# Optimization experiments

Measured on AMD Instinct MI355X. Metric: run time of the kernel, lower is better.

## Reference

```python
import jax, jax.numpy as jnp
import numpy as np

B, T, D, H, LAT = 512, 8, 512, 512, 64
NSTEPS = 4  # fixed RK4 steps per observation interval (replaces adaptive dopri5)


def _lin(key, out_dim, in_dim):
    k1, k2 = jax.random.split(key)
    s = 1.0 / np.sqrt(in_dim)
    W = jax.random.uniform(k1, (out_dim, in_dim), minval=-s, maxval=s, dtype=jnp.float32)
    b = jax.random.uniform(k2, (out_dim,), minval=-s, maxval=s, dtype=jnp.float32)
    return W, b


def setup_inputs() -> dict:
    key = jax.random.key(0)
    ks = jax.random.split(key, 8)
    x = jax.random.normal(ks[0], (B, T, D), dtype=jnp.float32)
    # strictly increasing per-sample observation times
    ts = jnp.cumsum(jax.random.uniform(ks[1], (B, T), dtype=jnp.float32) + 0.05, axis=1)
    Wih, bih = _lin(ks[2], 3 * H, D)      # GRU input weights
    Whh, bhh = _lin(ks[3], 3 * H, H)      # GRU hidden weights
    Wout, bout = _lin(ks[4], 2 * LAT, H)  # h2o head: mean/logvar of latent
    W1, b1 = _lin(ks[5], 2 * H, H + 1)    # LatentODEfunc fc1 (state + time)
    W2, b2 = _lin(ks[6], 2 * H, 2 * H)    # fc2
    W3, b3 = _lin(ks[7], H, 2 * H)        # fc3
    return dict(x=x, ts=ts, Wih=Wih, Whh=Whh, bih=bih, bhh=bhh,
                Wout=Wout, bout=bout, W1=W1, b1=b1, W2=W2, b2=b2, W3=W3, b3=b3)


def reference(x, ts, Wih, Whh, bih, bhh, Wout, bout, W1, b1, W2, b2, W3, b3):
    swish = lambda v: v * jax.nn.sigmoid(v)

    def odefunc(t, h):  # t: (B,), h: (B,H) -> dh/dt (B,H)
        z = jnp.concatenate([h, t[:, None]], axis=1)
        z = swish(z @ W1.T + b1)
        z = swish(z @ W2.T + b2)
        return z @ W3.T + b3

    def ode_integrate(h, t0, t1):  # batched RK4 with per-sample dt
        dt = (t1 - t0) / NSTEPS  # (B,)
        def body(carry, _):
            h, t = carry
            d = dt[:, None]
            k1 = odefunc(t, h)
            k2 = odefunc(t + dt / 2, h + d * k1 / 2)
            k3 = odefunc(t + dt / 2, h + d * k2 / 2)
            k4 = odefunc(t + dt, h + d * k3)
            return (h + d / 6 * (k1 + 2 * k2 + 2 * k3 + k4), t + dt), None
        (h, _), _ = jax.lax.scan(body, (h, t0), None, length=NSTEPS)
        return h

    def gru_cell(obs, h):  # torch GRUCell math
        gi = obs @ Wih.T + bih
        gh = h @ Whh.T + bhh
        ir, iz, inn = jnp.split(gi, 3, axis=1)
        hr, hz, hn = jnp.split(gh, 3, axis=1)
        r = jax.nn.sigmoid(ir + hr)
        zg = jax.nn.sigmoid(iz + hz)
        n = jnp.tanh(inn + r * hn)
        return (1.0 - zg) * n + zg * h

    # first interval has zero length -> RK4 with dt=0 leaves h0 unchanged (no ODE at t=0)
    t_prev = jnp.concatenate([ts[:, :1], ts[:, :-1]], axis=1)

    def step(carry, inputs):
        h, c = carry
        obs, t0, t1 = inputs
        h = ode_integrate(h, t0, t1)
        h = gru_cell(obs, h)
        out = h @ Wout.T + bout  # (B, 2*LAT)
        return (h, c), out

    h0 = jnp.zeros((x.shape[0], H), x.dtype)
    c0 = jnp.zeros_like(h0)
    xs = (jnp.swapaxes(x, 0, 1), t_prev.T, ts.T)  # time-major for scan
    (h, c), outs = jax.lax.scan(step, (h0, c0), xs)
    return outs[-1], h, c
```

## Files before the change

### kernel.cpp

```cpp
#include <hip/hip_runtime.h>
#include <hip/hip_bf16.h>
#include <stdint.h>


#define B_ 512
#define T_ 8
#define H_ 512
#define D_ 512

typedef short short8 __attribute__((ext_vector_type(8)));
typedef float f32x4 __attribute__((ext_vector_type(4)));
typedef __hip_bfloat16 bf16;
typedef unsigned long long u64;

__device__ __forceinline__ float sigm(float x){ return 1.f/(1.f+__expf(-x)); }

#define MFMA16(a,b,c) __builtin_amdgcn_mfma_f32_16x16x32_bf16((a),(b),(c),0,0,0)
#define ALD4(p)   __hip_atomic_load((p), __ATOMIC_RELAXED, __HIP_MEMORY_SCOPE_AGENT)
#define AST8(p,v) __hip_atomic_store((u64*)(p),(v),__ATOMIC_RELAXED,__HIP_MEMORY_SCOPE_AGENT)

__device__ __forceinline__ void wait_ge(unsigned* c, unsigned tgt, int* dead){
  if (threadIdx.x == 0){
    if (!*dead){
      int it = 0;
      while (ALD4(c) < tgt){
        __builtin_amdgcn_s_sleep(1);
        if (++it > 50000000){ *dead = 1; break; }
      }
    }
  }
  __syncthreads();
}
__device__ __forceinline__ void publish(unsigned* c){
  __builtin_amdgcn_s_waitcnt(0);
  __syncthreads();
  if (threadIdx.x == 0)
    __hip_atomic_fetch_add(c, 1u, __ATOMIC_RELAXED, __HIP_MEMORY_SCOPE_AGENT);
}

template<int CH, int SH>
__device__ __forceinline__ void stageC16(bf16* lds, int lstr, const bf16* g, int gstr){
  f32x4 tmp[CH];
#pragma unroll
  for (int j = 0; j < CH; ++j){
    int idx = j*256 + threadIdx.x;
    const bf16* p = g + (size_t)(idx >> SH)*gstr + (size_t)(idx & ((1<<SH)-1))*8;
    asm volatile("global_load_dwordx4 %0, %1, off sc0 sc1" : "=v"(tmp[j]) : "v"(p));
  }
  asm volatile("s_waitcnt vmcnt(0)" ::: "memory");
  __builtin_amdgcn_sched_barrier(0);
#pragma unroll
  for (int j = 0; j < CH; ++j){
    int idx = j*256 + threadIdx.x;
    *(f32x4*)&lds[(idx >> SH)*lstr + (idx & ((1<<SH)-1))*8] = tmp[j];
  }
}
template<int CH, int SH>
__device__ __forceinline__ void stageP(bf16* lds, int lstr, const bf16* g, size_t gstr){
#pragma unroll
  for (int j = 0; j < CH; ++j){
    int idx = j*256 + threadIdx.x;
    *(short8*)&lds[(idx >> SH)*lstr + (idx & ((1<<SH)-1))*8] =
        *(const short8*)(g + (size_t)(idx >> SH)*gstr + (size_t)(idx & ((1<<SH)-1))*8);
  }
}

__device__ __forceinline__ u64 pk4(float a0, float a1, float a2, float a3){
  union { bf16 h[4]; u64 q; } u;
  u.h[0] = __float2bfloat16(a0); u.h[1] = __float2bfloat16(a1);
  u.h[2] = __float2bfloat16(a2); u.h[3] = __float2bfloat16(a3);
  return u.q;
}

__global__ __launch_bounds__(256, 1) void persist_k(
    const bf16* __restrict__ W1hb, const bf16* __restrict__ W2b,
    const bf16* __restrict__ W3b,  const bf16* __restrict__ Woutb,
    const bf16* __restrict__ Wc3,  const bf16* __restrict__ xbf,
    const float* __restrict__ b1,  const float* __restrict__ b2,
    const float* __restrict__ b3,  const float* __restrict__ bout,
    const float* __restrict__ bcb3,const float* __restrict__ w1t,
    const float* __restrict__ ts,
    bf16* wbuf, bf16* z1buf, bf16* z2buf,
    unsigned* cnts, float* dout)
{
  extern __shared__ char smem[];
  bf16* slab = (bf16*)smem;
  bf16* W3s  = (bf16*)(smem + 66048);
  float* t0s = (float*)(smem + 132096);
  float* dts = t0s + 32;
  float* tcs = dts + 32;
  int* dead  = (int*)(smem + 132480);

  const int tid = threadIdx.x, lane = tid & 63, wv = tid >> 6;
  const int fr = lane & 15, quad = lane >> 4;
  const int nb = blockIdx.x & 15;
  const int mb = blockIdx.x >> 4;
  const int gm0 = mb * 32;
  const int wm = wv & 1;
  const int wn = wv >> 1;

  unsigned* cz1 = cnts + mb*128;
  unsigned* cz2 = cz1 + 32;
  unsigned* cw  = cz1 + 64;
  unsigned* cgt = cz1 + 96;

  stageP<16,7>(W3s, 1032, W3b + (size_t)(32*nb)*1024, 1024);
  if (tid < 32){
    float t0 = ts[(gm0 + tid)*T_];
    t0s[tid] = t0; tcs[tid] = t0; dts[tid] = 0.f;
  }
  if (tid == 0) *dead = 0;
  __syncthreads();

  const int zc0 = 64*nb + 16*wv + quad*4;
  const int kc0 = 32*nb + 16*wn + quad*4;
  const f32x4 b1v  = *(const f32x4*)&b1[zc0];
  const f32x4 w1tv = *(const f32x4*)&w1t[zc0];
  const f32x4 b2v  = *(const f32x4*)&b2[zc0];
  const f32x4 b3v  = *(const f32x4*)&b3[kc0];
  f32x4 bcv[4];
#pragma unroll
  for (int g = 0; g < 4; ++g)
    bcv[g] = *(const f32x4*)&bcb3[nb*128 + g*32 + 16*wn + quad*4];
  const f32x4 bov = *(const f32x4*)&bout[16*(nb & 7) + quad*4];

  const bf16* w1p = W1hb  + (size_t)(64*nb + 16*wv + fr)*512  + quad*8;
  const bf16* w2p = W2b   + (size_t)(64*nb + 16*wv + fr)*1024 + quad*8;
  const bf16* wop = Woutb + (size_t)(16*(nb & 7) + fr)*512 + quad*8;
  const bf16* wcp[4];
#pragma unroll
  for (int g = 0; g < 4; ++g)
    wcp[g] = Wc3 + (size_t)(nb*128 + g*32 + 16*wn + fr)*1024 + quad*8;

  short8 w1f[16], w2f[32];
#pragma unroll
  for (int k = 0; k < 16; ++k) w1f[k] = *(const short8*)(w1p + k*32);
#pragma unroll
  for (int k = 0; k < 32; ++k) w2f[k] = *(const short8*)(w2p + k*32);

  float hreg[4] = {0,0,0,0}, kacc[4] = {0,0,0,0};
  unsigned tz1 = 16, tz2 = 16, tw = 16, tg = 16;

  for (int s = 0; s < T_; ++s){
    for (int sub = 0; sub < 4; ++sub){
      for (int e = 1; e <= 4; ++e){
        wait_ge(cw, tw, dead);
        stageC16<8,6>(slab, 520, wbuf + (size_t)gm0*512, 512);
        __syncthreads();
        {
          f32x4 a0 = {0,0,0,0}, a1 = {0,0,0,0};
#pragma unroll
          for (int k = 0; k < 16; ++k){
            a0 = MFMA16(w1f[k], *(const short8*)&slab[fr*520      + k*32 + quad*8], a0);
            a1 = MFMA16(w1f[k], *(const short8*)&slab[(16+fr)*520 + k*32 + quad*8], a1);
          }
          float t0v = tcs[fr], t1v = tcs[16 + fr];
          float s0[4], s1[4];
#pragma unroll
          for (int j = 0; j < 4; ++j){
            float v0 = a0[j] + b1v[j] + t0v*w1tv[j];
            float v1 = a1[j] + b1v[j] + t1v*w1tv[j];
            s0[j] = v0*sigm(v0); s1[j] = v1*sigm(v1);
          }
          AST8(z1buf + (size_t)(gm0 + fr)*1024 + zc0,      pk4(s0[0],s0[1],s0[2],s0[3]));
          AST8(z1buf + (size_t)(gm0 + 16 + fr)*1024 + zc0, pk4(s1[0],s1[1],s1[2],s1[3]));
          publish(cz1);
        }
        wait_ge(cz1, tz1, dead); tz1 += 16;
        stageC16<16,7>(slab, 1032, z1buf + (size_t)gm0*1024, 1024);
        __syncthreads();
        {
          f32x4 a0 = {0,0,0,0}, a1 = {0,0,0,0};
#pragma unroll
          for (int k = 0; k < 32; ++k){
            a0 = MFMA16(w2f[k], *(const short8*)&slab[fr*1032      + k*32 + quad*8], a0);
            a1 = MFMA16(w2f[k], *(const short8*)&slab[(16+fr)*1032 + k*32 + quad*8], a1);
          }
          float s0[4], s1[4];
#pragma unroll
          for (int j = 0; j < 4; ++j){
            float v0 = a0[j] + b2v[j], v1 = a1[j] + b2v[j];
            s0[j] = v0*sigm(v0); s1[j] = v1*sigm(v1);
          }
          AST8(z2buf + (size_t)(gm0 + fr)*1024 + zc0,      pk4(s0[0],s0[1],s0[2],s0[3]));
          AST8(z2buf + (size_t)(gm0 + 16 + fr)*1024 + zc0, pk4(s1[0],s1[1],s1[2],s1[3]));
          publish(cz2);
        }
        wait_ge(cz2, tz2, dead); tz2 += 16;
        stageC16<16,7>(slab, 1032, z2buf + (size_t)gm0*1024, 1024);
        __syncthreads();
        {
          f32x4 ak = {0,0,0,0};
#pragma unroll 8
          for (int k = 0; k < 32; ++k){
            ak = MFMA16(*(const short8*)&W3s[(16*wn + fr)*1032 + k*32 + quad*8],
                        *(const short8*)&slab[(wm*16 + fr)*1032 + k*32 + quad*8], ak);
          }
          const int r = wm*16 + fr;
          const float dtv = dts[r];
          float w4[4];
#pragma unroll
          for (int j = 0; j < 4; ++j){
            float v = ak[j] + b3v[j];
            float ka = (e == 1) ? v : kacc[j] + ((e == 4) ? 1.f : 2.f)*v;
            if (e < 4){ kacc[j] = ka; w4[j] = hreg[j] + ((e == 3) ? 1.f : 0.5f)*dtv*v; }
            else      { hreg[j] = hreg[j] + dtv*(1.f/6.f)*ka; w4[j] = hreg[j]; }
          }
          AST8(wbuf + (size_t)(gm0 + r)*512 + kc0, pk4(w4[0],w4[1],w4[2],w4[3]));
          if (tid < 32){
            float ce = (e <= 2) ? ((float)sub + 0.5f) : ((float)sub + 1.f);
            tcs[tid] = t0s[tid] + dts[tid]*ce;
          }
          publish(cw); tw += 16;
        }
      }
    }
    wait_ge(cw, tw, dead);
    stageC16<8,6>(slab, 1032, wbuf + (size_t)gm0*512, 512);
    stageP<8,6>(slab + 512, 1032, xbf + ((size_t)gm0*T_ + s)*512, (size_t)T_*512);
    __syncthreads();
    publish(cgt);
    {
      f32x4 ag[4] = {{0,0,0,0},{0,0,0,0},{0,0,0,0},{0,0,0,0}};
#pragma unroll 4
      for (int k = 0; k < 32; ++k){
        short8 xv = *(const short8*)&slab[(wm*16 + fr)*1032 + k*32 + quad*8];
#pragma unroll
        for (int g = 0; g < 4; ++g)
          ag[g] = MFMA16(*(const short8*)(wcp[g] + k*32), xv, ag[g]);
      }
      wait_ge(cgt, tg, dead); tg += 16;
      const int r = wm*16 + fr;
#pragma unroll
      for (int j = 0; j < 4; ++j){
        float r_ = sigm(ag[0][j] + bcv[0][j]);
        float z_ = sigm(ag[1][j] + bcv[1][j]);
        float hn = ag[2][j] + bcv[2][j];
        float in = ag[3][j] + bcv[3][j];
        float n_ = tanhf(in + r_*hn);
        hreg[j] = (1.f - z_)*n_ + z_*hreg[j];
      }
      AST8(wbuf + (size_t)(gm0 + r)*512 + kc0, pk4(hreg[0],hreg[1],hreg[2],hreg[3]));
      if (tid < 32){
        float t0n = ts[(gm0 + tid)*T_ + s];
        float t1  = (s < T_-1) ? ts[(gm0 + tid)*T_ + s + 1] : t0n;
        t0s[tid] = t0n; tcs[tid] = t0n; dts[tid] = (t1 - t0n)*0.25f;
      }
      publish(cw); tw += 16;
    }
  }
  wait_ge(cw, tw, dead);
  stageC16<8,6>(slab, 520, wbuf + (size_t)gm0*512, 512);
  __syncthreads();
  if (nb < 8 && wv < 2){
    f32x4 ao = {0,0,0,0};
#pragma unroll 4
    for (int k = 0; k < 16; ++k){
      ao = MFMA16(*(const short8*)(wop + k*32),
                  *(const short8*)&slab[(wv*16 + fr)*520 + k*32 + quad*8], ao);
    }
    f32x4 o;
#pragma unroll
    for (int j = 0; j < 4; ++j) o[j] = ao[j] + bov[j];
    *(f32x4*)&dout[(size_t)(gm0 + wv*16 + fr)*128 + 16*nb + quad*4] = o;
  }
  {
    const int r = wm*16 + fr;
    f32x4 hv; hv[0]=hreg[0]; hv[1]=hreg[1]; hv[2]=hreg[2]; hv[3]=hreg[3];
    *(f32x4*)&dout[(size_t)B_*128 + (size_t)(gm0 + r)*512 + kc0] = hv;
    f32x4 z4 = {0,0,0,0};
    *(f32x4*)&dout[(size_t)B_*128 + (size_t)B_*512 + (size_t)(gm0 + r)*512 + kc0] = z4;
  }
}

__global__ void conv_k(const float* __restrict__ in, bf16* __restrict__ out,
                       int rows, int kin, int kout)
{
  int idx = blockIdx.x*256 + threadIdx.x;
  if (idx >= rows*kout) return;
  int r = idx / kout, k = idx - r*kout;
  out[idx] = __float2bfloat16(k < kin ? in[(size_t)r*kin + k] : 0.f);
}

__global__ void w1t_k(const float* __restrict__ W1, float* __restrict__ w1t)
{
  int i = blockIdx.x*256 + threadIdx.x;
  if (i < 1024) w1t[i] = W1[(size_t)i*513 + 512];
}

__global__ void wc3_k(const float* __restrict__ Wih, const float* __restrict__ Whh,
                      const float* __restrict__ bih, const float* __restrict__ bhh,
                      bf16* __restrict__ Wc3, float* __restrict__ bcb3)
{
  int idx = blockIdx.x*256 + threadIdx.x;
  if (idx >= 2048*1024) return;
  int R = idx >> 10, k = idx & 1023;
  int n16 = R >> 7, g = (R >> 5) & 3, c = R & 31;
  int hc = n16*32 + c;
  float v;
  if      (g == 0) v = (k < 512) ? Whh[(size_t)hc*512 + k]        : Wih[(size_t)hc*512 + k - 512];
  else if (g == 1) v = (k < 512) ? Whh[(size_t)(512+hc)*512 + k]  : Wih[(size_t)(512+hc)*512 + k - 512];
  else if (g == 2) v = (k < 512) ? Whh[(size_t)(1024+hc)*512 + k] : 0.f;
  else             v = (k < 512) ? 0.f                             : Wih[(size_t)(1024+hc)*512 + k - 512];
  Wc3[idx] = __float2bfloat16(v);
  if (k == 0){
    if      (g == 0) bcb3[R] = bih[hc] + bhh[hc];
    else if (g == 1) bcb3[R] = bih[512 + hc] + bhh[512 + hc];
    else if (g == 2) bcb3[R] = bhh[1024 + hc];
    else             bcb3[R] = bih[1024 + hc];
  }
}

__global__ void init_k(bf16* __restrict__ wbuf, unsigned* __restrict__ cnts)
{
  int idx = blockIdx.x*256 + threadIdx.x;
  if (idx < B_*H_) wbuf[idx] = __float2bfloat16(0.f);
  if (idx < 16*128){
    int off = idx & 127;
    cnts[idx] = (off == 64) ? 16u : 0u;
  }
}

extern "C" void kernel_launch(void* const* d_in, const int* in_sizes, int n_in,
                              void* d_out, int out_size, void* d_ws, size_t ws_size,
                              hipStream_t stream)
{
  const float* x    = (const float*)d_in[0];
  const float* ts   = (const float*)d_in[1];
  const float* Wih  = (const float*)d_in[2];
  const float* Whh  = (const float*)d_in[3];
  const float* bih  = (const float*)d_in[4];
  const float* bhh  = (const float*)d_in[5];
  const float* Wout = (const float*)d_in[6];
  const float* bout = (const float*)d_in[7];
  const float* W1   = (const float*)d_in[8];
  const float* b1   = (const float*)d_in[9];
  const float* W2   = (const float*)d_in[10];
  const float* b2   = (const float*)d_in[11];
  const float* W3   = (const float*)d_in[12];
  const float* b3   = (const float*)d_in[13];

  char* ws = (char*)d_ws;
  size_t off = 0;
  auto alloc = [&](size_t n){ void* p = ws + off; off += (n + 255) & ~(size_t)255; return p; };

  bf16* xbf   = (bf16*)alloc((size_t)B_*T_*D_*2);
  bf16* W1hb  = (bf16*)alloc((size_t)1024*512*2);
  bf16* W2b   = (bf16*)alloc((size_t)1024*1024*2);
  bf16* W3b   = (bf16*)alloc((size_t)512*1024*2);
  bf16* Woutb = (bf16*)alloc((size_t)128*512*2);
  bf16* Wc3   = (bf16*)alloc((size_t)2048*1024*2);
  float* bcb3 = (float*)alloc((size_t)2048*4);
  float* w1t  = (float*)alloc((size_t)1024*4);
  bf16* wbuf  = (bf16*)alloc((size_t)B_*H_*2);
  bf16* z1buf = (bf16*)alloc((size_t)B_*1024*2);
  bf16* z2buf = (bf16*)alloc((size_t)B_*1024*2);
  unsigned* cnts = (unsigned*)alloc((size_t)16*128*4);

  auto conv = [&](const float* in, bf16* out, int rows, int kin, int kout){
    int n = rows*kout;
    conv_k<<<(n + 255)/256, 256, 0, stream>>>(in, out, rows, kin, kout);
  };
  conv(x, xbf, B_*T_, D_, D_);
  conv(W1, W1hb, 1024, 513, 512);
  conv(W2, W2b, 1024, 1024, 1024);
  conv(W3, W3b, 512, 1024, 1024);
  conv(Wout, Woutb, 128, 512, 512);
  w1t_k<<<4, 256, 0, stream>>>(W1, w1t);
  wc3_k<<<(2048*1024)/256, 256, 0, stream>>>(Wih, Whh, bih, bhh, Wc3, bcb3);
  init_k<<<(B_*H_ + 255)/256, 256, 0, stream>>>(wbuf, cnts);

  (void)hipFuncSetAttribute((const void*)persist_k,
                            hipFuncAttributeMaxDynamicSharedMemorySize, 132608);
  persist_k<<<256, 256, 132608, stream>>>(
      W1hb, W2b, W3b, Woutb, Wc3, xbf,
      b1, b2, b3, bout, bcb3, w1t, ts,
      wbuf, z1buf, z2buf, cnts, (float*)d_out);
}
```

Before: 1.903 ms.

## Fold W3 into W1 so each RK4 stage chains fc2 to fused Wf=W1·W3

Precomputes Wf = W1[:, :H]·W3 and bf3 = W1·b3 so the next stage's fc1 pre-activation comes straight from z2 via one GEMM, removing the separate fc3 GEMM and its grid-wide sync phase per RK4 stage. The h state is tracked in fc1-projected space, and fc3 is applied once per interval to the weighted z2 sum. This cuts the barrier phases per stage from three to two but makes the per-stage GEMM K=1024 instead of 512, uses more register-resident weights, and changes bf16 rounding paths, which may affect accuracy.

```diff
diff --git a/kernel.cpp b/kernel.cpp
--- a/kernel.cpp
+++ b/kernel.cpp
@@ -74,22 +74,21 @@
 
 __global__ __launch_bounds__(256, 1) void persist_k(
     const bf16* __restrict__ W1hb, const bf16* __restrict__ W2b,
-    const bf16* __restrict__ W3b,  const bf16* __restrict__ Woutb,
-    const bf16* __restrict__ Wc3,  const bf16* __restrict__ xbf,
+    const bf16* __restrict__ Wfb,  const bf16* __restrict__ W3b,
+    const bf16* __restrict__ Woutb,const bf16* __restrict__ Wc3,
+    const bf16* __restrict__ xbf,
     const float* __restrict__ b1,  const float* __restrict__ b2,
     const float* __restrict__ b3,  const float* __restrict__ bout,
     const float* __restrict__ bcb3,const float* __restrict__ w1t,
-    const float* __restrict__ ts,
-    bf16* wbuf, bf16* z1buf, bf16* z2buf,
+    const float* __restrict__ bf3, const float* __restrict__ ts,
+    bf16* wbuf, bf16* hbuf, bf16* z1buf, bf16* z2buf, bf16* zbuf,
     unsigned* cnts, float* dout)
 {
   extern __shared__ char smem[];
   bf16* slab = (bf16*)smem;
-  bf16* W3s  = (bf16*)(smem + 66048);
-  float* t0s = (float*)(smem + 132096);
-  float* dts = t0s + 32;
-  float* tcs = dts + 32;
-  int* dead  = (int*)(smem + 132480);
+  float* t0s = (float*)(smem + 66048);
+  float* dts = (float*)(smem + 66176);
+  int* dead  = (int*)(smem + 66304);
 
   const int tid = threadIdx.x, lane = tid & 63, wv = tid >> 6;
   const int fr = lane & 15, quad = lane >> 4;
@@ -101,13 +100,12 @@
 
   unsigned* cz1 = cnts + mb*128;
   unsigned* cz2 = cz1 + 32;
-  unsigned* cw  = cz1 + 64;
-  unsigned* cgt = cz1 + 96;
-
-  stageP<16,7>(W3s, 1032, W3b + (size_t)(32*nb)*1024, 1024);
+  unsigned* ch  = cz1 + 64;
+  unsigned* cg  = cz1 + 96;
+
   if (tid < 32){
     float t0 = ts[(gm0 + tid)*T_];
-    t0s[tid] = t0; tcs[tid] = t0; dts[tid] = 0.f;
+    t0s[tid] = t0; dts[tid] = 0.f;
   }
   if (tid == 0) *dead = 0;
   __syncthreads();
@@ -117,6 +115,7 @@
   const f32x4 b1v  = *(const f32x4*)&b1[zc0];
   const f32x4 w1tv = *(const f32x4*)&w1t[zc0];
   const f32x4 b2v  = *(const f32x4*)&b2[zc0];
+  const f32x4 bf3v = *(const f32x4*)&bf3[zc0];
   const f32x4 b3v  = *(const f32x4*)&b3[kc0];
   f32x4 bcv[4];
 #pragma unroll
@@ -126,46 +125,43 @@
 
   const bf16* w1p = W1hb  + (size_t)(64*nb + 16*wv + fr)*512  + quad*8;
   const bf16* w2p = W2b   + (size_t)(64*nb + 16*wv + fr)*1024 + quad*8;
+  const bf16* wfp = Wfb   + (size_t)(64*nb + 16*wv + fr)*1024 + quad*8;
+  const bf16* w3p = W3b   + (size_t)(32*nb + 16*wn + fr)*1024 + quad*8;
   const bf16* wop = Woutb + (size_t)(16*(nb & 7) + fr)*512 + quad*8;
   const bf16* wcp[4];
 #pragma unroll
   for (int g = 0; g < 4; ++g)
     wcp[g] = Wc3 + (size_t)(nb*128 + g*32 + 16*wn + fr)*1024 + quad*8;
 
-  short8 w1f[16], w2f[32];
-#pragma unroll
-  for (int k = 0; k < 16; ++k) w1f[k] = *(const short8*)(w1p + k*32);
+  short8 w2f[32], wff[32];
 #pragma unroll
   for (int k = 0; k < 32; ++k) w2f[k] = *(const short8*)(w2p + k*32);
-
-  float hreg[4] = {0,0,0,0}, kacc[4] = {0,0,0,0};
-  unsigned tz1 = 16, tz2 = 16, tw = 16, tg = 16;
+#pragma unroll
+  for (int k = 0; k < 32; ++k) wff[k] = *(const short8*)(wfp + k*32);
+
+  float hw0[4]={0,0,0,0}, hw1[4]={0,0,0,0};
+  float pacc0[4]={0,0,0,0}, pacc1[4]={0,0,0,0};
+  float zacc0[4]={0,0,0,0}, zacc1[4]={0,0,0,0};
+  float hreg[4]={0,0,0,0};
+  unsigned tz1 = 16, tz2 = 16, tch = 16, tcg = 16;
+
+  {
+    const float t0a = t0s[fr], t0b = t0s[16 + fr];
+    float v0[4], v1[4];
+#pragma unroll
+    for (int j = 0; j < 4; ++j){
+      v0[j] = t0a*w1tv[j] + b1v[j];
+      v1[j] = t0b*w1tv[j] + b1v[j];
+      v0[j] *= sigm(v0[j]); v1[j] *= sigm(v1[j]);
+    }
+    AST8(z1buf + (size_t)(gm0 + fr)*1024 + zc0,      pk4(v0[0],v0[1],v0[2],v0[3]));
+    AST8(z1buf + (size_t)(gm0 + 16 + fr)*1024 + zc0, pk4(v1[0],v1[1],v1[2],v1[3]));
+    publish(cz1);
+  }
 
   for (int s = 0; s < T_; ++s){
     for (int sub = 0; sub < 4; ++sub){
       for (int e = 1; e <= 4; ++e){
-        wait_ge(cw, tw, dead);
-        stageC16<8,6>(slab, 520, wbuf + (size_t)gm0*512, 512);
-        __syncthreads();
-        {
-          f32x4 a0 = {0,0,0,0}, a1 = {0,0,0,0};
-#pragma unroll
-          for (int k = 0; k < 16; ++k){
-            a0 = MFMA16(w1f[k], *(const short8*)&slab[fr*520      + k*32 + quad*8], a0);
-            a1 = MFMA16(w1f[k], *(const short8*)&slab[(16+fr)*520 + k*32 + quad*8], a1);
-          }
-          float t0v = tcs[fr], t1v = tcs[16 + fr];
-          float s0[4], s1[4];
-#pragma unroll
-          for (int j = 0; j < 4; ++j){
-            float v0 = a0[j] + b1v[j] + t0v*w1tv[j];
-            float v1 = a1[j] + b1v[j] + t1v*w1tv[j];
-            s0[j] = v0*sigm(v0); s1[j] = v1*sigm(v1);
-          }
-          AST8(z1buf + (size_t)(gm0 + fr)*1024 + zc0,      pk4(s0[0],s0[1],s0[2],s0[3]));
-          AST8(z1buf + (size_t)(gm0 + 16 + fr)*1024 + zc0, pk4(s1[0],s1[1],s1[2],s1[3]));
-          publish(cz1);
-        }
         wait_ge(cz1, tz1, dead); tz1 += 16;
         stageC16<16,7>(slab, 1032, z1buf + (size_t)gm0*1024, 1024);
         __syncthreads();
@@ -176,50 +172,92 @@
             a0 = MFMA16(w2f[k], *(const short8*)&slab[fr*1032      + k*32 + quad*8], a0);
             a1 = MFMA16(w2f[k], *(const short8*)&slab[(16+fr)*1032 + k*32 + quad*8], a1);
           }
+          const float wgt = (e == 2 || e == 3) ? 2.f : 1.f;
           float s0[4], s1[4];
 #pragma unroll
           for (int j = 0; j < 4; ++j){
             float v0 = a0[j] + b2v[j], v1 = a1[j] + b2v[j];
             s0[j] = v0*sigm(v0); s1[j] = v1*sigm(v1);
+            zacc0[j] += wgt*s0[j]; zacc1[j] += wgt*s1[j];
           }
-          AST8(z2buf + (size_t)(gm0 + fr)*1024 + zc0,      pk4(s0[0],s0[1],s0[2],s0[3]));
-          AST8(z2buf + (size_t)(gm0 + 16 + fr)*1024 + zc0, pk4(s1[0],s1[1],s1[2],s1[3]));
+          if (sub == 3 && e == 4){
+            AST8(zbuf + (size_t)(gm0 + fr)*1024 + zc0,      pk4(zacc0[0],zacc0[1],zacc0[2],zacc0[3]));
+            AST8(zbuf + (size_t)(gm0 + 16 + fr)*1024 + zc0, pk4(zacc1[0],zacc1[1],zacc1[2],zacc1[3]));
+#pragma unroll
+            for (int j = 0; j < 4; ++j){ zacc0[j] = 0.f; zacc1[j] = 0.f; }
+          } else {
+            AST8(z2buf + (size_t)(gm0 + fr)*1024 + zc0,      pk4(s0[0],s0[1],s0[2],s0[3]));
+            AST8(z2buf + (size_t)(gm0 + 16 + fr)*1024 + zc0, pk4(s1[0],s1[1],s1[2],s1[3]));
+          }
           publish(cz2);
         }
-        wait_ge(cz2, tz2, dead); tz2 += 16;
-        stageC16<16,7>(slab, 1032, z2buf + (size_t)gm0*1024, 1024);
-        __syncthreads();
-        {
-          f32x4 ak = {0,0,0,0};
+        if (!(sub == 3 && e == 4)){
+          wait_ge(cz2, tz2, dead); tz2 += 16;
+          stageC16<16,7>(slab, 1032, z2buf + (size_t)gm0*1024, 1024);
+          __syncthreads();
+          f32x4 p0 = {0,0,0,0}, p1 = {0,0,0,0};
+#pragma unroll
+          for (int k = 0; k < 32; ++k){
+            p0 = MFMA16(wff[k], *(const short8*)&slab[fr*1032      + k*32 + quad*8], p0);
+            p1 = MFMA16(wff[k], *(const short8*)&slab[(16+fr)*1032 + k*32 + quad*8], p1);
+          }
+          const float dta = dts[fr], dtb = dts[16 + fr];
+          const float t0a = t0s[fr], t0b = t0s[16 + fr];
+          const float ce = (e <= 2) ? (float)sub + 0.5f : (float)sub + 1.f;
+          float v0[4], v1[4];
+          if (e < 4){
+            const float c = (e == 3) ? 1.f : 0.5f;
+            const float wgt = (e == 2 || e == 3) ? 2.f : 1.f;
+            if (sub < 3){
+#pragma unroll
+              for (int j = 0; j < 4; ++j){ pacc0[j] += wgt*p0[j]; pacc1[j] += wgt*p1[j]; }
+            }
+#pragma unroll
+            for (int j = 0; j < 4; ++j){
+              v0[j] = hw0[j] + c*dta*(p0[j] + bf3v[j]) + (t0a + dta*ce)*w1tv[j] + b1v[j];
+              v1[j] = hw1[j] + c*dtb*(p1[j] + bf3v[j]) + (t0b + dtb*ce)*w1tv[j] + b1v[j];
+            }
+          } else {
+#pragma unroll
+            for (int j = 0; j < 4; ++j){
+              float pa = pacc0[j] + p0[j], pb = pacc1[j] + p1[j];
+              hw0[j] += dta*(1.f/6.f)*pa + dta*bf3v[j];
+              hw1[j] += dtb*(1.f/6.f)*pb + dtb*bf3v[j];
+              pacc0[j] = 0.f; pacc1[j] = 0.f;
+              v0[j] = hw0[j] + (t0a + dta*ce)*w1tv[j] + b1v[j];
+              v1[j] = hw1[j] + (t0b + dtb*ce)*w1tv[j] + b1v[j];
+            }
+          }
+#pragma unroll
+          for (int j = 0; j < 4; ++j){ v0[j] *= sigm(v0[j]); v1[j] *= sigm(v1[j]); }
+          AST8(z1buf + (size_t)(gm0 + fr)*1024 + zc0,      pk4(v0[0],v0[1],v0[2],v0[3]));
+          AST8(z1buf + (size_t)(gm0 + 16 + fr)*1024 + zc0, pk4(v1[0],v1[1],v1[2],v1[3]));
+          publish(cz1);
+        }
+      }
+    }
+    wait_ge(cz2, tz2, dead); tz2 += 16;
+    stageC16<16,7>(slab, 1032, zbuf + (size_t)gm0*1024, 1024);
+    __syncthreads();
+    {
+      f32x4 ak = {0,0,0,0};
 #pragma unroll 8
-          for (int k = 0; k < 32; ++k){
-            ak = MFMA16(*(const short8*)&W3s[(16*wn + fr)*1032 + k*32 + quad*8],
-                        *(const short8*)&slab[(wm*16 + fr)*1032 + k*32 + quad*8], ak);
-          }
-          const int r = wm*16 + fr;
-          const float dtv = dts[r];
-          float w4[4];
-#pragma unroll
-          for (int j = 0; j < 4; ++j){
-            float v = ak[j] + b3v[j];
-            float ka = (e == 1) ? v : kacc[j] + ((e == 4) ? 1.f : 2.f)*v;
-            if (e < 4){ kacc[j] = ka; w4[j] = hreg[j] + ((e == 3) ? 1.f : 0.5f)*dtv*v; }
-            else      { hreg[j] = hreg[j] + dtv*(1.f/6.f)*ka; w4[j] = hreg[j]; }
-          }
-          AST8(wbuf + (size_t)(gm0 + r)*512 + kc0, pk4(w4[0],w4[1],w4[2],w4[3]));
-          if (tid < 32){
-            float ce = (e <= 2) ? ((float)sub + 0.5f) : ((float)sub + 1.f);
-            tcs[tid] = t0s[tid] + dts[tid]*ce;
-          }
-          publish(cw); tw += 16;
-        }
-      }
-    }
-    wait_ge(cw, tw, dead);
-    stageC16<8,6>(slab, 1032, wbuf + (size_t)gm0*512, 512);
+      for (int k = 0; k < 32; ++k){
+        ak = MFMA16(*(const short8*)(w3p + k*32),
+                    *(const short8*)&slab[(wm*16 + fr)*1032 + k*32 + quad*8], ak);
+      }
+      const int r = wm*16 + fr;
+      const float dtv = dts[r];
+#pragma unroll
+      for (int j = 0; j < 4; ++j)
+        hreg[j] = hreg[j] + dtv*(1.f/6.f)*ak[j] + 4.f*dtv*b3v[j];
+      AST8(hbuf + (size_t)(gm0 + r)*512 + kc0, pk4(hreg[0],hreg[1],hreg[2],hreg[3]));
+      publish(ch);
+    }
+    wait_ge(ch, tch, dead); tch += 16;
+    stageC16<8,6>(slab, 1032, hbuf + (size_t)gm0*512, 512);
     stageP<8,6>(slab + 512, 1032, xbf + ((size_t)gm0*T_ + s)*512, (size_t)T_*512);
     __syncthreads();
-    publish(cgt);
     {
       f32x4 ag[4] = {{0,0,0,0},{0,0,0,0},{0,0,0,0},{0,0,0,0}};
 #pragma unroll 4
@@ -229,7 +267,6 @@
         for (int g = 0; g < 4; ++g)
           ag[g] = MFMA16(*(const short8*)(wcp[g] + k*32), xv, ag[g]);
       }
-      wait_ge(cgt, tg, dead); tg += 16;
       const int r = wm*16 + fr;
 #pragma unroll
       for (int j = 0; j < 4; ++j){
@@ -241,15 +278,45 @@
         hreg[j] = (1.f - z_)*n_ + z_*hreg[j];
       }
       AST8(wbuf + (size_t)(gm0 + r)*512 + kc0, pk4(hreg[0],hreg[1],hreg[2],hreg[3]));
+      if (s == T_-1){
+        f32x4 hv; hv[0]=hreg[0]; hv[1]=hreg[1]; hv[2]=hreg[2]; hv[3]=hreg[3];
+        *(f32x4*)&dout[(size_t)B_*128 + (size_t)(gm0 + r)*512 + kc0] = hv;
+        f32x4 z4 = {0,0,0,0};
+        *(f32x4*)&dout[(size_t)B_*128 + (size_t)B_*512 + (size_t)(gm0 + r)*512 + kc0] = z4;
+      }
       if (tid < 32){
         float t0n = ts[(gm0 + tid)*T_ + s];
         float t1  = (s < T_-1) ? ts[(gm0 + tid)*T_ + s + 1] : t0n;
-        t0s[tid] = t0n; tcs[tid] = t0n; dts[tid] = (t1 - t0n)*0.25f;
-      }
-      publish(cw); tw += 16;
-    }
-  }
-  wait_ge(cw, tw, dead);
+        t0s[tid] = t0n; dts[tid] = (t1 - t0n)*0.25f;
+      }
+      publish(cg);
+    }
+    if (s < T_-1){
+      wait_ge(cg, tcg, dead); tcg += 16;
+      stageC16<8,6>(slab, 520, wbuf + (size_t)gm0*512, 512);
+      __syncthreads();
+      f32x4 a0 = {0,0,0,0}, a1 = {0,0,0,0};
+#pragma unroll 4
+      for (int k = 0; k < 16; ++k){
+        short8 wt = *(const short8*)(w1p + k*32);
+        a0 = MFMA16(wt, *(const short8*)&slab[fr*520      + k*32 + quad*8], a0);
+        a1 = MFMA16(wt, *(const short8*)&slab[(16+fr)*520 + k*32 + quad*8], a1);
+      }
+      const float t0a = t0s[fr], t0b = t0s[16 + fr];
+      float v0[4], v1[4];
+#pragma unroll
+      for (int j = 0; j < 4; ++j){
+        hw0[j] = a0[j]; hw1[j] = a1[j];
+        v0[j] = hw0[j] + t0a*w1tv[j] + b1v[j];
+        v1[j] = hw1[j] + t0b*w1tv[j] + b1v[j];
+        v0[j] *= sigm(v0[j]); v1[j] *= sigm(v1[j]);
+      }
+      AST8(z1buf + (size_t)(gm0 + fr)*1024 + zc0,      pk4(v0[0],v0[1],v0[2],v0[3]));
+      AST8(z1buf + (size_t)(gm0 + 16 + fr)*1024 + zc0, pk4(v1[0],v1[1],v1[2],v1[3]));
+      publish(cz1);
+    }
+  }
+  wait_ge(cg, tcg, dead); tcg += 16;
   stageC16<8,6>(slab, 520, wbuf + (size_t)gm0*512, 512);
   __syncthreads();
   if (nb < 8 && wv < 2){
@@ -264,13 +331,6 @@
     for (int j = 0; j < 4; ++j) o[j] = ao[j] + bov[j];
     *(f32x4*)&dout[(size_t)(gm0 + wv*16 + fr)*128 + 16*nb + quad*4] = o;
   }
-  {
-    const int r = wm*16 + fr;
-    f32x4 hv; hv[0]=hreg[0]; hv[1]=hreg[1]; hv[2]=hreg[2]; hv[3]=hreg[3];
-    *(f32x4*)&dout[(size_t)B_*128 + (size_t)(gm0 + r)*512 + kc0] = hv;
-    f32x4 z4 = {0,0,0,0};
-    *(f32x4*)&dout[(size_t)B_*128 + (size_t)B_*512 + (size_t)(gm0 + r)*512 + kc0] = z4;
-  }
 }
 
 __global__ void conv_k(const float* __restrict__ in, bf16* __restrict__ out,
@@ -286,6 +346,56 @@
 {
   int i = blockIdx.x*256 + threadIdx.x;
   if (i < 1024) w1t[i] = W1[(size_t)i*513 + 512];
+}
+
+__global__ void wf_k(const float* __restrict__ W1, const float* __restrict__ W3,
+                     bf16* __restrict__ Wfb)
+{
+  __shared__ float At[64][64];
+  __shared__ float Bt[64][65];
+  const int i0 = blockIdx.y*64, j0 = blockIdx.x*64;
+  const int tid = threadIdx.x;
+  const int ty = tid >> 4, tx = tid & 15;
+  float acc[4][4] = {};
+  for (int kc = 0; kc < 512; kc += 64){
+#pragma unroll
+    for (int t = 0; t < 16; ++t){
+      int idx = t*256 + tid;
+      int r = idx >> 6, k = idx & 63;
+      At[r][k] = W1[(size_t)(i0 + r)*513 + kc + k];
+      Bt[r][k] = W3[(size_t)(kc + r)*1024 + j0 + k];
+    }
+    __syncthreads();
+#pragma unroll 8
+    for (int k = 0; k < 64; ++k){
+      float a[4], b[4];
+#pragma unroll
+      for (int ii = 0; ii < 4; ++ii) a[ii] = At[ty*4 + ii][k];
+#pragma unroll
+      for (int jj = 0; jj < 4; ++jj) b[jj] = Bt[k][tx*4 + jj];
+#pragma unroll
+      for (int ii = 0; ii < 4; ++ii)
+#pragma unroll
+        for (int jj = 0; jj < 4; ++jj) acc[ii][jj] += a[ii]*b[jj];
+    }
+    __syncthreads();
+  }
+#pragma unroll
+  for (int ii = 0; ii < 4; ++ii)
+#pragma unroll
+    for (int jj = 0; jj < 4; ++jj)
+      Wfb[(size_t)(i0 + ty*4 + ii)*1024 + j0 + tx*4 + jj] = __float2bfloat16(acc[ii][jj]);
+}
+
+__global__ void bf3_k(const float* __restrict__ W1, const float* __restrict__ b3,
+                      float* __restrict__ bf3)
+{
+  int i = blockIdx.x*256 + threadIdx.x;
+  if (i < 1024){
+    float acc = 0.f;
+    for (int c = 0; c < 512; ++c) acc += W1[(size_t)i*513 + c]*b3[c];
+    bf3[i] = acc;
+  }
 }
 
 __global__ void wc3_k(const float* __restrict__ Wih, const float* __restrict__ Whh,
@@ -311,14 +421,10 @@
   }
 }
 
-__global__ void init_k(bf16* __restrict__ wbuf, unsigned* __restrict__ cnts)
+__global__ void init_k(unsigned* __restrict__ cnts)
 {
   int idx = blockIdx.x*256 + threadIdx.x;
-  if (idx < B_*H_) wbuf[idx] = __float2bfloat16(0.f);
-  if (idx < 16*128){
-    int off = idx & 127;
-    cnts[idx] = (off == 64) ? 16u : 0u;
-  }
+  if (idx < 16*128) cnts[idx] = 0u;
 }
 
 extern "C" void kernel_launch(void* const* d_in, const int* in_sizes, int n_in,
@@ -347,14 +453,18 @@
   bf16* xbf   = (bf16*)alloc((size_t)B_*T_*D_*2);
   bf16* W1hb  = (bf16*)alloc((size_t)1024*512*2);
   bf16* W2b   = (bf16*)alloc((size_t)1024*1024*2);
+  bf16* Wfb   = (bf16*)alloc((size_t)1024*1024*2);
   bf16* W3b   = (bf16*)alloc((size_t)512*1024*2);
   bf16* Woutb = (bf16*)alloc((size_t)128*512*2);
   bf16* Wc3   = (bf16*)alloc((size_t)2048*1024*2);
   float* bcb3 = (float*)alloc((size_t)2048*4);
   float* w1t  = (float*)alloc((size_t)1024*4);
+  float* bf3  = (float*)alloc((size_t)1024*4);
   bf16* wbuf  = (bf16*)alloc((size_t)B_*H_*2);
+  bf16* hbuf  = (bf16*)alloc((size_t)B_*H_*2);
   bf16* z1buf = (bf16*)alloc((size_t)B_*1024*2);
   bf16* z2buf = (bf16*)alloc((size_t)B_*1024*2);
+  bf16* zbuf  = (bf16*)alloc((size_t)B_*1024*2);
   unsigned* cnts = (unsigned*)alloc((size_t)16*128*4);
 
   auto conv = [&](const float* in, bf16* out, int rows, int kin, int kout){
@@ -367,13 +477,15 @@
   conv(W3, W3b, 512, 1024, 1024);
   conv(Wout, Woutb, 128, 512, 512);
   w1t_k<<<4, 256, 0, stream>>>(W1, w1t);
+  wf_k<<<dim3(16,16), 256, 0, stream>>>(W1, W3, Wfb);
+  bf3_k<<<4, 256, 0, stream>>>(W1, b3, bf3);
   wc3_k<<<(2048*1024)/256, 256, 0, stream>>>(Wih, Whh, bih, bhh, Wc3, bcb3);
-  init_k<<<(B_*H_ + 255)/256, 256, 0, stream>>>(wbuf, cnts);
+  init_k<<<8, 256, 0, stream>>>(cnts);
 
   (void)hipFuncSetAttribute((const void*)persist_k,
-                            hipFuncAttributeMaxDynamicSharedMemorySize, 132608);
-  persist_k<<<256, 256, 132608, stream>>>(
-      W1hb, W2b, W3b, Woutb, Wc3, xbf,
-      b1, b2, b3, bout, bcb3, w1t, ts,
-      wbuf, z1buf, z2buf, cnts, (float*)d_out);
-}
+                            hipFuncAttributeMaxDynamicSharedMemorySize, 66560);
+  persist_k<<<256, 256, 66560, stream>>>(
+      W1hb, W2b, Wfb, W3b, Woutb, Wc3, xbf,
+      b1, b2, b3, bout, bcb3, w1t, bf3, ts,
+      wbuf, hbuf, z1buf, z2buf, zbuf, cnts, (float*)d_out);
+}
```

New measurement: 1.822 ms. 4.2% less time.
